# Optimization experiments

Measured on AMD Instinct MI355X. Metric: run time of the kernel, lower is better.

Reference implementation:

```python
import jax, jax.numpy as jnp
import numpy as np

DIM = 1024
HID = 4096
NH = 16
HD = DIM // NH
B, S = 4, 2048
EPS = 1e-5
NEG = -1e9  # stand-in for -inf causal mask fill (numerically safe)


def layer_norm(x, g, b):
    mu = jnp.mean(x, axis=-1, keepdims=True)
    var = jnp.mean((x - mu) ** 2, axis=-1, keepdims=True)
    return (x - mu) * jax.lax.rsqrt(var + EPS) * g + b


def setup_inputs() -> dict:
    key = jax.random.key(0)
    ks = jax.random.split(key, 8)
    x = jax.random.normal(ks[0], (B, S, DIM), dtype=jnp.float32)
    # causal additive mask, broadcastable to [B, NH, S, S]
    causal = jnp.tril(jnp.ones((S, S), dtype=bool))
    mask = jnp.where(causal, 0.0, NEG).astype(jnp.float32)[None, None]
    sc = 1.0 / np.sqrt(DIM)
    wq = jax.random.normal(ks[1], (DIM, DIM), dtype=jnp.float32) * sc
    wk = jax.random.normal(ks[2], (DIM, DIM), dtype=jnp.float32) * sc
    wv = jax.random.normal(ks[3], (DIM, DIM), dtype=jnp.float32) * sc
    wo = jax.random.normal(ks[4], (DIM, DIM), dtype=jnp.float32) * sc
    w1 = jax.random.normal(ks[5], (DIM, HID), dtype=jnp.float32) * sc
    w2 = jax.random.normal(ks[6], (HID, DIM), dtype=jnp.float32) * (1.0 / np.sqrt(HID))
    ln1_w = jnp.ones((DIM,), jnp.float32); ln1_b = jnp.zeros((DIM,), jnp.float32)
    ln2_w = jnp.ones((DIM,), jnp.float32); ln2_b = jnp.zeros((DIM,), jnp.float32)
    return {"x": x, "mask": mask, "wq": wq, "wk": wk, "wv": wv, "wo": wo,
            "w1": w1, "w2": w2, "ln1_w": ln1_w, "ln1_b": ln1_b,
            "ln2_w": ln2_w, "ln2_b": ln2_b}


def reference(x, mask, wq, wk, wv, wo, w1, w2, ln1_w, ln1_b, ln2_w, ln2_b):
    b, s, _ = x.shape
    # pre-norm attention
    xn = layer_norm(x, ln1_w, ln1_b)
    q = (xn @ wq).reshape(b, s, NH, HD)
    k = (xn @ wk).reshape(b, s, NH, HD)
    v = (xn @ wv).reshape(b, s, NH, HD)
    scores = jnp.einsum('bqhd,bkhd->bhqk', q, k) / np.sqrt(HD) + mask
    probs = jax.nn.softmax(scores.astype(jnp.float32), axis=-1).astype(x.dtype)
    attn = jnp.einsum('bhqk,bkhd->bqhd', probs, v).reshape(b, s, NH * HD)
    h = x + attn @ wo
    # pre-norm ReLU FFN
    hn = layer_norm(h, ln2_w, ln2_b)
    ff = jax.nn.relu((hn @ w1).astype(jnp.float32)).astype(x.dtype) @ w2
    return h + ff
```

## Files before the change

kernel.cpp:

```cpp
#include <hip/hip_runtime.h>
#include <hip/hip_bf16.h>
#include <type_traits>

#define DIM 1024
#define HID 4096
#define NH 16
#define HD 64
#define BB 4
#define SS 2048
#define NROW (BB*SS)

typedef __attribute__((ext_vector_type(8))) short short8;
typedef __attribute__((ext_vector_type(4))) short short4v;
typedef __attribute__((ext_vector_type(4))) float f32x4;

__device__ __forceinline__ void gload16(const void* src, void* lds) {
  __builtin_amdgcn_global_load_lds(
      (const __attribute__((address_space(1))) unsigned int*)src,
      (__attribute__((address_space(3))) unsigned int*)lds, 16, 0, 0);
}
__device__ __forceinline__ short f2b(float f) {
  return __builtin_bit_cast(short, __float2bfloat16(f));
}
__device__ __forceinline__ float b2f(short s) {
  return __uint_as_float(((unsigned)(unsigned short)s) << 16);
}

__global__ __launch_bounds__(256) void ln_k(const float* __restrict__ x,
                                            const float* __restrict__ g,
                                            const float* __restrict__ bta,
                                            short* __restrict__ out) {
  int row = blockIdx.x;
  int t = threadIdx.x;
  int lane = t & 63, wid = t >> 6;
  float4 v = *(const float4*)(x + (size_t)row*DIM + t*4);
  float f[4] = {v.x, v.y, v.z, v.w};
  float s1 = 0.f, s2 = 0.f;
#pragma unroll
  for (int j = 0; j < 4; j++) { s1 += f[j]; s2 += f[j]*f[j]; }
#pragma unroll
  for (int off = 32; off > 0; off >>= 1) { s1 += __shfl_xor(s1, off); s2 += __shfl_xor(s2, off); }
  __shared__ float red[8];
  if (lane == 0) { red[wid] = s1; red[4+wid] = s2; }
  __syncthreads();
  s1 = red[0]+red[1]+red[2]+red[3];
  s2 = red[4]+red[5]+red[6]+red[7];
  float mu = s1 * (1.0f/DIM);
  float var = s2 * (1.0f/DIM) - mu*mu;
  float rs = rsqrtf(var + 1e-5f);
  float4 gv = *(const float4*)(g + t*4);
  float4 bv = *(const float4*)(bta + t*4);
  short4v o;
  o[0] = f2b((f[0]-mu)*rs*gv.x + bv.x);
  o[1] = f2b((f[1]-mu)*rs*gv.y + bv.y);
  o[2] = f2b((f[2]-mu)*rs*gv.z + bv.z);
  o[3] = f2b((f[3]-mu)*rs*gv.w + bv.w);
  *(short4v*)(out + (size_t)row*DIM + t*4) = o;
}

__global__ __launch_bounds__(256) void transp_f2b(const float* __restrict__ in, short* __restrict__ out,
                                                  int R, int C) {
  __shared__ __align__(16) short tile[64][72];
  int r0 = blockIdx.x*64, c0 = blockIdx.y*64;
  int t = threadIdx.x;
  int cr = t >> 4;
  int cc4 = (t & 15) * 4;
#pragma unroll
  for (int i = 0; i < 4; i++) {
    float4 v = *(const float4*)(in + (size_t)(r0 + cr + i*16)*C + c0 + cc4);
    tile[cr + i*16][cc4 + 0] = f2b(v.x);
    tile[cr + i*16][cc4 + 1] = f2b(v.y);
    tile[cr + i*16][cc4 + 2] = f2b(v.z);
    tile[cr + i*16][cc4 + 3] = f2b(v.w);
  }
  __syncthreads();
  int rr = t >> 3, cc = (t & 7) * 8;
#pragma unroll
  for (int i = 0; i < 2; i++) {
    int oc = rr + i*32;
    short8 v;
#pragma unroll
    for (int j = 0; j < 8; j++) v[j] = tile[cc + j][oc];
    *(short8*)(out + (size_t)(c0 + oc)*R + r0 + cc) = v;
  }
}

__global__ __launch_bounds__(256) void vtrans(const short* __restrict__ qkv, short* __restrict__ vt) {
  __shared__ __align__(16) short tile[64][72];
  int s0 = blockIdx.x*64;
  int z = blockIdx.y; int b = z >> 4, h = z & 15;
  int t = threadIdx.x;
  int rr = t >> 3, cc = (t & 7) * 8;
#pragma unroll
  for (int i = 0; i < 2; i++) {
    short8 v = *(const short8*)(qkv + (size_t)(b*SS + s0 + rr + i*32)*(3*DIM) + 2*DIM + h*HD + cc);
    *(short8*)&tile[rr + i*32][cc] = v;
  }
  __syncthreads();
#pragma unroll
  for (int i = 0; i < 2; i++) {
    int d = rr + i*32;
    short8 v;
#pragma unroll
    for (int j = 0; j < 8; j++) v[j] = tile[cc + j][d];
    *(short8*)(vt + ((size_t)z*HD + d)*SS + s0 + cc) = v;
  }
}

template<int EPI, typename CT>
__global__ __launch_bounds__(512) void gemm_bt(const short* __restrict__ A, int lda,
                                               const short* __restrict__ Bt, int ldb,
                                               CT* C, int ldc,
                                               const float* Res, int ldr,
                                               int K) {
  __shared__ __align__(16) short ldsA[128*64];
  __shared__ __align__(16) short ldsB[128*64];
  int t = threadIdx.x, lane = t & 63, wid = t >> 6;
  int bm = blockIdx.x*128, bn = blockIdx.y*128;
  int wr = wid >> 2, wc = wid & 3;
  f32x4 z4 = {0.f, 0.f, 0.f, 0.f};
  f32x4 acc[4][2];
#pragma unroll
  for (int m = 0; m < 4; m++)
#pragma unroll
    for (int n = 0; n < 2; n++) acc[m][n] = z4;
  const int srcCol = (((t & 7) ^ ((t >> 3) & 7)) * 8);
  const short* pa = A + (size_t)(bm + (t >> 3))*lda + srcCol;
  const short* pb = Bt + (size_t)(bn + (t >> 3))*ldb + srcCol;
  const int rowXor = (lane & 7) << 3;
  for (int k0 = 0; k0 < K; k0 += 64) {
    gload16(pa,                   &ldsA[wid*512]);
    gload16(pa + (size_t)64*lda,  &ldsA[4096 + wid*512]);
    gload16(pb,                   &ldsB[wid*512]);
    gload16(pb + (size_t)64*ldb,  &ldsB[4096 + wid*512]);
    pa += 64; pb += 64;
    __syncthreads();
    short8 af[4][2], bfr[2][2];
#pragma unroll
    for (int m = 0; m < 4; m++) {
      int row = wr*64 + m*16 + (lane & 15);
#pragma unroll
      for (int kk = 0; kk < 2; kk++)
        af[m][kk] = *(const short8*)&ldsA[row*64 + ((kk*32 + (lane >> 4)*8) ^ rowXor)];
    }
#pragma unroll
    for (int n = 0; n < 2; n++) {
      int row = wc*32 + n*16 + (lane & 15);
#pragma unroll
      for (int kk = 0; kk < 2; kk++)
        bfr[n][kk] = *(const short8*)&ldsB[row*64 + ((kk*32 + (lane >> 4)*8) ^ rowXor)];
    }
#pragma unroll
    for (int m = 0; m < 4; m++)
#pragma unroll
      for (int n = 0; n < 2; n++)
#pragma unroll
        for (int kk = 0; kk < 2; kk++)
          acc[m][n] = __builtin_amdgcn_mfma_f32_16x16x32_bf16(af[m][kk], bfr[n][kk], acc[m][n], 0, 0, 0);
    __syncthreads();
  }
#pragma unroll
  for (int m = 0; m < 4; m++) {
    int r0 = bm + wr*64 + m*16 + ((lane >> 4) << 2);
#pragma unroll
    for (int n = 0; n < 2; n++) {
      int c = bn + wc*32 + n*16 + (lane & 15);
#pragma unroll
      for (int r = 0; r < 4; r++) {
        float v = acc[m][n][r];
        if constexpr (EPI == 1) v = fmaxf(v, 0.0f);
        if constexpr (EPI == 3) v += Res[(size_t)(r0 + r)*ldr + c];
        if constexpr (std::is_same<CT, float>::value)
          C[(size_t)(r0 + r)*ldc + c] = v;
        else
          C[(size_t)(r0 + r)*ldc + c] = f2b(v);
      }
    }
  }
}

__global__ __launch_bounds__(256) void attn_k(short* qkv, const short* __restrict__ vt) {
  __shared__ __align__(16) short ldsK[2][64*64];
  __shared__ __align__(16) short ldsV[2][64*64];
  __shared__ __align__(16) short ldsP[4][2*16*64];
  int t = threadIdx.x, lane = t & 63, wid = t >> 6;
  int wgid = blockIdx.x;
  int xcd = wgid & 7, idx = wgid >> 3;
  int z  = xcd*8 + (idx & 7);
  int qi = 15 - (idx >> 3);
  int q0 = qi*128;
  int b = z >> 4, h = z & 15;
  const int ld = 3*DIM;
  const float SCALE2 = 0.125f * 1.44269504f;
  const float THR2   = 8.0f * 1.44269504f;
  short8 qf[2][2];
#pragma unroll
  for (int m = 0; m < 2; m++) {
    const short* qp = qkv + (size_t)(b*SS + q0 + m*64 + wid*16 + (lane & 15))*ld + h*HD + (lane >> 4)*8;
    qf[m][0] = *(const short8*)qp;
    qf[m][1] = *(const short8*)(qp + 32);
  }
  f32x4 z4 = {0.f, 0.f, 0.f, 0.f};
  f32x4 accO[2][4];
#pragma unroll
  for (int m = 0; m < 2; m++)
#pragma unroll
    for (int n = 0; n < 4; n++) accO[m][n] = z4;
  float m_r[2][4], lp[2][4];
#pragma unroll
  for (int m = 0; m < 2; m++)
#pragma unroll
    for (int r = 0; r < 4; r++) { m_r[m][r] = -1e30f; lp[m][r] = 0.f; }
  const int srcCol = (((lane & 7) ^ (lane >> 3)) * 8);
  const int rowXor = (lane & 7) << 3;
  int ntiles = 2*qi + 2;

  auto STAGE = [&](int it, int bsel) {
    int kv0 = it*64;
    const short* sk = qkv + (size_t)(b*SS + kv0 + (t >> 3))*ld + DIM + h*HD + srcCol;
    gload16(sk,                  &ldsK[bsel][wid*512]);
    gload16(sk + (size_t)32*ld,  &ldsK[bsel][2048 + wid*512]);
    const short* sv = vt + ((size_t)z*HD + (t >> 3))*SS + kv0 + srcCol;
    gload16(sv,                  &ldsV[bsel][wid*512]);
    gload16(sv + (size_t)32*SS,  &ldsV[bsel][2048 + wid*512]);
  };

  STAGE(0, 0);
  __syncthreads();
  for (int it = 0; it < ntiles; ++it) {
    int cur = it & 1;
    if (it + 1 < ntiles) STAGE(it + 1, cur ^ 1);
    int kv0 = it*64;
    f32x4 sacc[2][4];
#pragma unroll
    for (int m = 0; m < 2; m++)
#pragma unroll
      for (int n = 0; n < 4; n++) sacc[m][n] = z4;
    __builtin_amdgcn_s_setprio(1);
#pragma unroll
    for (int n = 0; n < 4; n++) {
#pragma unroll
      for (int kk = 0; kk < 2; kk++) {
        int colK = (kk*32 + (lane >> 4)*8) ^ rowXor;
        short8 kb = *(const short8*)&ldsK[cur][(n*16 + (lane & 15))*64 + colK];
#pragma unroll
        for (int m = 0; m < 2; m++)
          if (it <= 2*qi + m)
            sacc[m][n] = __builtin_amdgcn_mfma_f32_16x16x32_bf16(qf[m][kk], kb, sacc[m][n], 0, 0, 0);
      }
    }
    __builtin_amdgcn_s_setprio(0);
#pragma unroll
    for (int m = 0; m < 2; m++) {
      if (it > 2*qi + m) continue;
      if (it == 2*qi + m) {
#pragma unroll
        for (int n = 0; n < 4; n++) {
          int kg = kv0 + n*16 + (lane & 15);
#pragma unroll
          for (int r = 0; r < 4; r++) {
            int qg = q0 + m*64 + wid*16 + ((lane >> 4) << 2) + r;
            sacc[m][n][r] = (kg <= qg) ? sacc[m][n][r] : -1e30f;
          }
        }
      }
      float mxs[4];
      float dmax = -1e30f;
#pragma unroll
      for (int r = 0; r < 4; r++) {
        float mx = fmaxf(fmaxf(sacc[m][0][r], sacc[m][1][r]), fmaxf(sacc[m][2][r], sacc[m][3][r]));
#pragma unroll
        for (int off = 1; off < 16; off <<= 1) mx = fmaxf(mx, __shfl_xor(mx, off));
        mxs[r] = mx * SCALE2;
        dmax = fmaxf(dmax, mxs[r] - m_r[m][r]);
      }
      if (__any(dmax > THR2)) {
#pragma unroll
        for (int r = 0; r < 4; r++) {
          float mn = fmaxf(m_r[m][r], mxs[r]);
          float al = exp2f(m_r[m][r] - mn);
          m_r[m][r] = mn;
          lp[m][r] *= al;
#pragma unroll
          for (int n = 0; n < 4; n++) accO[m][n][r] *= al;
        }
      }
#pragma unroll
      for (int r = 0; r < 4; r++) {
        float mn = m_r[m][r];
        float rs = 0.f;
#pragma unroll
        for (int n = 0; n < 4; n++) {
          float p = exp2f(fmaf(sacc[m][n][r], SCALE2, -mn));
          sacc[m][n][r] = p;
          rs += p;
        }
        lp[m][r] += rs;
      }
#pragma unroll
      for (int n = 0; n < 4; n++)
#pragma unroll
        for (int r = 0; r < 4; r++) {
          int prow = ((lane >> 4) << 2) + r;
          int pcol = (n*16 + (lane & 15)) ^ ((prow & 7) << 3);
          ldsP[wid][m*1024 + prow*64 + pcol] = f2b(sacc[m][n][r]);
        }
    }
    __builtin_amdgcn_s_setprio(1);
#pragma unroll
    for (int nn = 0; nn < 4; nn++) {
#pragma unroll
      for (int kk = 0; kk < 2; kk++) {
        int colP = (kk*32 + (lane >> 4)*8) ^ rowXor;
        short8 vb = *(const short8*)&ldsV[cur][(nn*16 + (lane & 15))*64 + colP];
#pragma unroll
        for (int m = 0; m < 2; m++)
          if (it <= 2*qi + m) {
            short8 pfr = *(const short8*)&ldsP[wid][m*1024 + (lane & 15)*64 + colP];
            accO[m][nn] = __builtin_amdgcn_mfma_f32_16x16x32_bf16(pfr, vb, accO[m][nn], 0, 0, 0);
          }
      }
    }
    __builtin_amdgcn_s_setprio(0);
    __syncthreads();
  }
#pragma unroll
  for (int m = 0; m < 2; m++) {
    float rl[4];
#pragma unroll
    for (int r = 0; r < 4; r++) {
      float l = lp[m][r];
#pragma unroll
      for (int off = 1; off < 16; off <<= 1) l += __shfl_xor(l, off);
      rl[r] = 1.0f / l;
    }
#pragma unroll
    for (int nn = 0; nn < 4; nn++) {
#pragma unroll
      for (int r = 0; r < 4; r++) {
        int qg = q0 + m*64 + wid*16 + ((lane >> 4) << 2) + r;
        float ov = accO[m][nn][r] * rl[r];
        qkv[(size_t)(b*SS + qg)*ld + 2*DIM + h*HD + nn*16 + (lane & 15)] = f2b(ov);
      }
    }
  }
}

extern "C" void kernel_launch(void* const* d_in, const int* in_sizes, int n_in,
                              void* d_out, int out_size, void* d_ws, size_t ws_size,
                              hipStream_t stream) {
  (void)in_sizes; (void)n_in; (void)out_size; (void)ws_size;
  const float* x    = (const float*)d_in[0];
  const float* wq   = (const float*)d_in[2];
  const float* wk   = (const float*)d_in[3];
  const float* wv   = (const float*)d_in[4];
  const float* wo   = (const float*)d_in[5];
  const float* w1   = (const float*)d_in[6];
  const float* w2   = (const float*)d_in[7];
  const float* ln1w = (const float*)d_in[8];
  const float* ln1b = (const float*)d_in[9];
  const float* ln2w = (const float*)d_in[10];
  const float* ln2b = (const float*)d_in[11];
  float* out = (float*)d_out;

  short* ws = (short*)d_ws;
  size_t o = 0;
  short* wqkvT = ws + o; o += (size_t)3*DIM*DIM;
  short* woT   = ws + o; o += (size_t)DIM*DIM;
  short* w1T   = ws + o; o += (size_t)HID*DIM;
  short* w2T   = ws + o; o += (size_t)DIM*HID;
  short* xn    = ws + o; o += (size_t)NROW*DIM;
  short* qkv   = ws + o; o += (size_t)NROW*3*DIM;
  short* ff1   = ws + o; o += (size_t)NROW*HID;
  short* vtb   = ff1;

  dim3 B256(256), B512(512);
  transp_f2b<<<dim3(16,16), B256, 0, stream>>>(wq, wqkvT,             DIM, DIM);
  transp_f2b<<<dim3(16,16), B256, 0, stream>>>(wk, wqkvT + DIM*DIM,   DIM, DIM);
  transp_f2b<<<dim3(16,16), B256, 0, stream>>>(wv, wqkvT + 2*DIM*DIM, DIM, DIM);
  transp_f2b<<<dim3(16,16), B256, 0, stream>>>(wo, woT, DIM, DIM);
  transp_f2b<<<dim3(16,64), B256, 0, stream>>>(w1, w1T, DIM, HID);
  transp_f2b<<<dim3(64,16), B256, 0, stream>>>(w2, w2T, HID, DIM);
  ln_k<<<NROW, B256, 0, stream>>>(x, ln1w, ln1b, xn);
  gemm_bt<0, short><<<dim3(NROW/128, 3*DIM/128), B512, 0, stream>>>(xn, DIM, wqkvT, DIM, qkv, 3*DIM, nullptr, 0, DIM);
  vtrans<<<dim3(SS/64, BB*NH), B256, 0, stream>>>(qkv, vtb);
  attn_k<<<dim3(1024), B256, 0, stream>>>(qkv, vtb);
  gemm_bt<3, float><<<dim3(NROW/128, DIM/128), B512, 0, stream>>>(qkv + 2*DIM, 3*DIM, woT, DIM, out, DIM, x, DIM, DIM);
  ln_k<<<NROW, B256, 0, stream>>>(out, ln2w, ln2b, xn);
  gemm_bt<1, short><<<dim3(NROW/128, HID/128), B512, 0, stream>>>(xn, DIM, w1T, DIM, ff1, HID, nullptr, 0, DIM);
  gemm_bt<3, float><<<dim3(NROW/128, DIM/128), B512, 0, stream>>>(ff1, HID, w2T, HID, out, DIM, out, DIM, HID);
}
```

Baseline: 449.7 us.

## Split attention block across eight waves, one 16-row query tile each

The attention kernel now launches 512 threads per block, and each of eight waves owns a single 16-row query slice instead of four waves each owning two slices. K/V staging is spread across twice as many threads with one load per thread, and per-wave registers (accumulators, Q fragments, softmax state) are halved. The aim is more latency hiding and lower register pressure per wave. The cost is that each K/V LDS tile is read by twice as many waves, the block-wide barrier now spans more waves, and the upper-half waves sit idle on the final diagonal tile.

```diff
diff --git a/kernel.cpp b/kernel.cpp
--- a/kernel.cpp
+++ b/kernel.cpp
@@ -179,10 +179,10 @@
   }
 }
 
-__global__ __launch_bounds__(256) void attn_k(short* qkv, const short* __restrict__ vt) {
+__global__ __launch_bounds__(512) void attn_k(short* qkv, const short* __restrict__ vt) {
   __shared__ __align__(16) short ldsK[2][64*64];
   __shared__ __align__(16) short ldsV[2][64*64];
-  __shared__ __align__(16) short ldsP[4][2*16*64];
+  __shared__ __align__(16) short ldsP[8][16*64];
   int t = threadIdx.x, lane = t & 63, wid = t >> 6;
   int wgid = blockIdx.x;
   int xcd = wgid & 7, idx = wgid >> 3;
@@ -193,36 +193,31 @@
   const int ld = 3*DIM;
   const float SCALE2 = 0.125f * 1.44269504f;
   const float THR2   = 8.0f * 1.44269504f;
-  short8 qf[2][2];
-#pragma unroll
-  for (int m = 0; m < 2; m++) {
-    const short* qp = qkv + (size_t)(b*SS + q0 + m*64 + wid*16 + (lane & 15))*ld + h*HD + (lane >> 4)*8;
-    qf[m][0] = *(const short8*)qp;
-    qf[m][1] = *(const short8*)(qp + 32);
+  const int half = wid >> 2;
+  const int myq = q0 + wid*16;
+  short8 qf[2];
+  {
+    const short* qp = qkv + (size_t)(b*SS + myq + (lane & 15))*ld + h*HD + (lane >> 4)*8;
+    qf[0] = *(const short8*)qp;
+    qf[1] = *(const short8*)(qp + 32);
   }
   f32x4 z4 = {0.f, 0.f, 0.f, 0.f};
-  f32x4 accO[2][4];
-#pragma unroll
-  for (int m = 0; m < 2; m++)
-#pragma unroll
-    for (int n = 0; n < 4; n++) accO[m][n] = z4;
-  float m_r[2][4], lp[2][4];
-#pragma unroll
-  for (int m = 0; m < 2; m++)
-#pragma unroll
-    for (int r = 0; r < 4; r++) { m_r[m][r] = -1e30f; lp[m][r] = 0.f; }
-  const int srcCol = (((lane & 7) ^ (lane >> 3)) * 8);
+  f32x4 accO[4];
+#pragma unroll
+  for (int n = 0; n < 4; n++) accO[n] = z4;
+  float m_r[4], lp[4];
+#pragma unroll
+  for (int r = 0; r < 4; r++) { m_r[r] = -1e30f; lp[r] = 0.f; }
+  const int srcCol = (((lane & 7) ^ ((lane >> 3) & 7)) * 8);
   const int rowXor = (lane & 7) << 3;
   int ntiles = 2*qi + 2;
 
   auto STAGE = [&](int it, int bsel) {
     int kv0 = it*64;
     const short* sk = qkv + (size_t)(b*SS + kv0 + (t >> 3))*ld + DIM + h*HD + srcCol;
-    gload16(sk,                  &ldsK[bsel][wid*512]);
-    gload16(sk + (size_t)32*ld,  &ldsK[bsel][2048 + wid*512]);
+    gload16(sk, &ldsK[bsel][wid*512]);
     const short* sv = vt + ((size_t)z*HD + (t >> 3))*SS + kv0 + srcCol;
-    gload16(sv,                  &ldsV[bsel][wid*512]);
-    gload16(sv + (size_t)32*SS,  &ldsV[bsel][2048 + wid*512]);
+    gload16(sv, &ldsV[bsel][wid*512]);
   };
 
   STAGE(0, 0);
@@ -231,36 +226,29 @@
     int cur = it & 1;
     if (it + 1 < ntiles) STAGE(it + 1, cur ^ 1);
     int kv0 = it*64;
-    f32x4 sacc[2][4];
-#pragma unroll
-    for (int m = 0; m < 2; m++)
-#pragma unroll
-      for (int n = 0; n < 4; n++) sacc[m][n] = z4;
-    __builtin_amdgcn_s_setprio(1);
-#pragma unroll
-    for (int n = 0; n < 4; n++) {
-#pragma unroll
-      for (int kk = 0; kk < 2; kk++) {
-        int colK = (kk*32 + (lane >> 4)*8) ^ rowXor;
-        short8 kb = *(const short8*)&ldsK[cur][(n*16 + (lane & 15))*64 + colK];
-#pragma unroll
-        for (int m = 0; m < 2; m++)
-          if (it <= 2*qi + m)
-            sacc[m][n] = __builtin_amdgcn_mfma_f32_16x16x32_bf16(qf[m][kk], kb, sacc[m][n], 0, 0, 0);
-      }
-    }
-    __builtin_amdgcn_s_setprio(0);
-#pragma unroll
-    for (int m = 0; m < 2; m++) {
-      if (it > 2*qi + m) continue;
-      if (it == 2*qi + m) {
+    if (it <= 2*qi + half) {
+      f32x4 sacc[4];
+#pragma unroll
+      for (int n = 0; n < 4; n++) sacc[n] = z4;
+      __builtin_amdgcn_s_setprio(1);
+#pragma unroll
+      for (int n = 0; n < 4; n++) {
+#pragma unroll
+        for (int kk = 0; kk < 2; kk++) {
+          int colK = (kk*32 + (lane >> 4)*8) ^ rowXor;
+          short8 kb = *(const short8*)&ldsK[cur][(n*16 + (lane & 15))*64 + colK];
+          sacc[n] = __builtin_amdgcn_mfma_f32_16x16x32_bf16(qf[kk], kb, sacc[n], 0, 0, 0);
+        }
+      }
+      __builtin_amdgcn_s_setprio(0);
+      if (it == 2*qi + half) {
 #pragma unroll
         for (int n = 0; n < 4; n++) {
           int kg = kv0 + n*16 + (lane & 15);
 #pragma unroll
           for (int r = 0; r < 4; r++) {
-            int qg = q0 + m*64 + wid*16 + ((lane >> 4) << 2) + r;
-            sacc[m][n][r] = (kg <= qg) ? sacc[m][n][r] : -1e30f;
+            int qg = myq + ((lane >> 4) << 2) + r;
+            sacc[n][r] = (kg <= qg) ? sacc[n][r] : -1e30f;
           }
         }
       }
@@ -268,34 +256,34 @@
       float dmax = -1e30f;
 #pragma unroll
       for (int r = 0; r < 4; r++) {
-        float mx = fmaxf(fmaxf(sacc[m][0][r], sacc[m][1][r]), fmaxf(sacc[m][2][r], sacc[m][3][r]));
+        float mx = fmaxf(fmaxf(sacc[0][r], sacc[1][r]), fmaxf(sacc[2][r], sacc[3][r]));
 #pragma unroll
         for (int off = 1; off < 16; off <<= 1) mx = fmaxf(mx, __shfl_xor(mx, off));
         mxs[r] = mx * SCALE2;
-        dmax = fmaxf(dmax, mxs[r] - m_r[m][r]);
+        dmax = fmaxf(dmax, mxs[r] - m_r[r]);
       }
       if (__any(dmax > THR2)) {
 #pragma unroll
         for (int r = 0; r < 4; r++) {
-          float mn = fmaxf(m_r[m][r], mxs[r]);
-          float al = exp2f(m_r[m][r] - mn);
-          m_r[m][r] = mn;
-          lp[m][r] *= al;
-#pragma unroll
-          for (int n = 0; n < 4; n++) accO[m][n][r] *= al;
+          float mn = fmaxf(m_r[r], mxs[r]);
+          float al = exp2f(m_r[r] - mn);
+          m_r[r] = mn;
+          lp[r] *= al;
+#pragma unroll
+          for (int n = 0; n < 4; n++) accO[n][r] *= al;
         }
       }
 #pragma unroll
       for (int r = 0; r < 4; r++) {
-        float mn = m_r[m][r];
+        float mn = m_r[r];
         float rs = 0.f;
 #pragma unroll
         for (int n = 0; n < 4; n++) {
-          float p = exp2f(fmaf(sacc[m][n][r], SCALE2, -mn));
-          sacc[m][n][r] = p;
+          float p = exp2f(fmaf(sacc[n][r], SCALE2, -mn));
+          sacc[n][r] = p;
           rs += p;
         }
-        lp[m][r] += rs;
+        lp[r] += rs;
       }
 #pragma unroll
       for (int n = 0; n < 4; n++)
@@ -303,33 +291,28 @@
         for (int r = 0; r < 4; r++) {
           int prow = ((lane >> 4) << 2) + r;
           int pcol = (n*16 + (lane & 15)) ^ ((prow & 7) << 3);
-          ldsP[wid][m*1024 + prow*64 + pcol] = f2b(sacc[m][n][r]);
-        }
-    }
-    __builtin_amdgcn_s_setprio(1);
-#pragma unroll
-    for (int nn = 0; nn < 4; nn++) {
-#pragma unroll
-      for (int kk = 0; kk < 2; kk++) {
-        int colP = (kk*32 + (lane >> 4)*8) ^ rowXor;
-        short8 vb = *(const short8*)&ldsV[cur][(nn*16 + (lane & 15))*64 + colP];
-#pragma unroll
-        for (int m = 0; m < 2; m++)
-          if (it <= 2*qi + m) {
-            short8 pfr = *(const short8*)&ldsP[wid][m*1024 + (lane & 15)*64 + colP];
-            accO[m][nn] = __builtin_amdgcn_mfma_f32_16x16x32_bf16(pfr, vb, accO[m][nn], 0, 0, 0);
-          }
-      }
-    }
-    __builtin_amdgcn_s_setprio(0);
+          ldsP[wid][prow*64 + pcol] = f2b(sacc[n][r]);
+        }
+      __builtin_amdgcn_s_setprio(1);
+#pragma unroll
+      for (int nn = 0; nn < 4; nn++) {
+#pragma unroll
+        for (int kk = 0; kk < 2; kk++) {
+          int colP = (kk*32 + (lane >> 4)*8) ^ rowXor;
+          short8 vb  = *(const short8*)&ldsV[cur][(nn*16 + (lane & 15))*64 + colP];
+          short8 pfr = *(const short8*)&ldsP[wid][(lane & 15)*64 + colP];
+          accO[nn] = __builtin_amdgcn_mfma_f32_16x16x32_bf16(pfr, vb, accO[nn], 0, 0, 0);
+        }
+      }
+      __builtin_amdgcn_s_setprio(0);
+    }
     __syncthreads();
   }
-#pragma unroll
-  for (int m = 0; m < 2; m++) {
+  {
     float rl[4];
 #pragma unroll
     for (int r = 0; r < 4; r++) {
-      float l = lp[m][r];
+      float l = lp[r];
 #pragma unroll
       for (int off = 1; off < 16; off <<= 1) l += __shfl_xor(l, off);
       rl[r] = 1.0f / l;
@@ -338,8 +321,8 @@
     for (int nn = 0; nn < 4; nn++) {
 #pragma unroll
       for (int r = 0; r < 4; r++) {
-        int qg = q0 + m*64 + wid*16 + ((lane >> 4) << 2) + r;
-        float ov = accO[m][nn][r] * rl[r];
+        int qg = myq + ((lane >> 4) << 2) + r;
+        float ov = accO[nn][r] * rl[r];
         qkv[(size_t)(b*SS + qg)*ld + 2*DIM + h*HD + nn*16 + (lane & 15)] = f2b(ov);
       }
     }
@@ -384,7 +367,7 @@
   ln_k<<<NROW, B256, 0, stream>>>(x, ln1w, ln1b, xn);
   gemm_bt<0, short><<<dim3(NROW/128, 3*DIM/128), B512, 0, stream>>>(xn, DIM, wqkvT, DIM, qkv, 3*DIM, nullptr, 0, DIM);
   vtrans<<<dim3(SS/64, BB*NH), B256, 0, stream>>>(qkv, vtb);
-  attn_k<<<dim3(1024), B256, 0, stream>>>(qkv, vtb);
+  attn_k<<<dim3(1024), B512, 0, stream>>>(qkv, vtb);
   gemm_bt<3, float><<<dim3(NROW/128, DIM/128), B512, 0, stream>>>(qkv + 2*DIM, 3*DIM, woT, DIM, out, DIM, x, DIM, DIM);
   ln_k<<<NROW, B256, 0, stream>>>(out, ln2w, ln2b, xn);
   gemm_bt<1, short><<<dim3(NROW/128, HID/128), B512, 0, stream>>>(xn, DIM, w1T, DIM, ff1, HID, nullptr, 0, DIM);
```

New measurement: 408.6 us. 1.1x faster.
